# Performance work log

Measured on AMD Instinct MI355X. Metric: run time of the kernel, lower is better.

Reference implementation:

```python
import jax, jax.numpy as jnp
import numpy as np

D_MODEL = 1024
N_HEADS = 16
D_HEAD = D_MODEL // N_HEADS  # 64
NUM_MEM_KV = 4
SCALE = D_HEAD ** -0.5


def setup_inputs() -> dict:
    key = jax.random.key(0)
    k1, k2, k3, k4 = jax.random.split(key, 4)
    x = jax.random.normal(k1, (4, 4096, D_MODEL), dtype=jnp.float32)
    mask = jax.random.randint(k2, (4, 4096), 0, 2).astype(jnp.int32)
    w_qkv = jax.random.normal(k3, (3 * D_MODEL, D_MODEL), dtype=jnp.float32) * 0.02
    mem_kv = jax.random.normal(k4, (2, N_HEADS, NUM_MEM_KV, D_HEAD), dtype=jnp.float32)
    return {"x": x, "w_qkv": w_qkv, "mem_kv": mem_kv, "mask": mask}


def reference(x, w_qkv, mem_kv, mask):
    b, l, _ = x.shape
    # qkv projection: nn.Linear applies x @ W^T; reshape matches torch view(..., h, d_head, 3)
    qkv = jnp.einsum('bld,ed->ble', x, w_qkv).reshape(b, l, N_HEADS, D_HEAD, 3)
    qkv = jnp.moveaxis(qkv, 2, 1)  # (b, h, l, d_head, 3)
    q, k, v = qkv[..., 0], qkv[..., 1], qkv[..., 2]

    m = mask.astype(x.dtype)[:, None, :, None]  # (b, 1, l, 1) per prepare_mask
    k = jnp.where(m == 0, -jnp.inf, k * m)

    # prepend learned memory kv along the sequence axis
    mk = jnp.broadcast_to(mem_kv[0], (b, N_HEADS, NUM_MEM_KV, D_HEAD))
    mv = jnp.broadcast_to(mem_kv[1], (b, N_HEADS, NUM_MEM_KV, D_HEAD))
    k = jnp.concatenate([mk, k], axis=-2)  # (b, h, m+l, d_head)
    v = jnp.concatenate([mv, v], axis=-2)

    q = jax.nn.softmax(q * SCALE, axis=-1)   # softmax over feature dim
    k = jax.nn.softmax(k, axis=-2)           # softmax over sequence dim; -inf rows -> 0 weight

    context = jnp.einsum('bhnd,bhne->bhde', k, v)   # (b, h, d_head, d_head)
    out = jnp.einsum('bhld,bhde->bhle', q, context)  # (b, h, l, d_head)
    out = out * m
    out = jnp.moveaxis(out, 1, 2).reshape(b, l, N_HEADS * D_HEAD)
    return out
```

## Files before the change

kernel.cpp:

```cpp
#include <hip/hip_runtime.h>

typedef _Float16 h8 __attribute__((ext_vector_type(8)));
typedef _Float16 h4 __attribute__((ext_vector_type(4)));
typedef float f4 __attribute__((ext_vector_type(4)));

typedef __attribute__((address_space(1))) const void GV;
typedef __attribute__((address_space(3))) void SV;

__device__ __forceinline__ void async16(const void* g, void* s) {
  __builtin_amdgcn_global_load_lds((GV*)g, (SV*)s, 16, 0, 0);
}


#define XC 2097152
#define WC 393216

__global__ __launch_bounds__(256) void cvt_f16(const float4* __restrict__ x,
                                               const float4* __restrict__ w,
                                               h8* __restrict__ xh,
                                               h8* __restrict__ wh) {
  int t = blockIdx.x * 256 + threadIdx.x;
  if (t < XC) {
    const int row = t >> 7, c7 = t & 127;
    const int dst = (row << 7) | (c7 & 120) | ((c7 & 7) ^ (row & 7));
    float4 a = x[t * 2], b = x[t * 2 + 1];
    h8 o = {(_Float16)a.x, (_Float16)a.y, (_Float16)a.z, (_Float16)a.w,
            (_Float16)b.x, (_Float16)b.y, (_Float16)b.z, (_Float16)b.w};
    xh[dst] = o;
  } else {
    const int u = t - XC;
    const int rp = u >> 7, c7 = u & 127;
    int sr;
    if (rp < 2048) {
      int h = rp >> 7, c = rp & 127;
      sr = h * 192 + ((c < 64) ? (c * 3 + 1) : ((c - 64) * 3 + 2));
    } else {
      int q = rp - 2048;
      sr = (q >> 6) * 192 + (q & 63) * 3;
    }
    const int dst = (rp << 7) | (c7 & 120) | ((c7 & 7) ^ (rp & 7));
    float4 a = w[sr * 256 + c7 * 2], b = w[sr * 256 + c7 * 2 + 1];
    h8 o = {(_Float16)a.x, (_Float16)a.y, (_Float16)a.z, (_Float16)a.w,
            (_Float16)b.x, (_Float16)b.y, (_Float16)b.z, (_Float16)b.w};
    wh[dst] = o;
  }
}


__device__ __forceinline__ void ld4(h8 (&dst)[2][4], const _Float16* buf, int rbase,
                                    int l15, int quad, int swz) {
#pragma unroll
  for (int ks = 0; ks < 2; ++ks) {
    const int pc = ((((ks << 2) | quad) ^ swz)) << 3;
#pragma unroll
    for (int i = 0; i < 4; ++i)
      dst[ks][i] = *(const h8*)&buf[(rbase + i * 16 + l15) * 64 + pc];
  }
}

__device__ __forceinline__ void ld2(h8 (&dst)[2][2], const _Float16* buf, int rbase,
                                    int l15, int quad, int swz) {
#pragma unroll
  for (int ks = 0; ks < 2; ++ks) {
    const int pc = ((((ks << 2) | quad) ^ swz)) << 3;
#pragma unroll
    for (int j = 0; j < 2; ++j)
      dst[ks][j] = *(const h8*)&buf[(rbase + j * 16 + l15) * 64 + pc];
  }
}

template <int MH, int NH>
__device__ __forceinline__ void mq(f4 (&acc)[8][4], const h8 (&af)[2][4],
                                   const h8 (&bf)[2][2]) {
#pragma unroll
  for (int ks = 0; ks < 2; ++ks)
#pragma unroll
    for (int i = 0; i < 4; ++i)
#pragma unroll
      for (int j = 0; j < 2; ++j)
        acc[MH * 4 + i][NH * 2 + j] = __builtin_amdgcn_mfma_f32_16x16x32_f16(
            af[ks][i], bf[ks][j], acc[MH * 4 + i][NH * 2 + j], 0, 0, 0);
}

__device__ __forceinline__ void stage(const _Float16* g, _Float16* l, int it, int tid) {
  async16(g + (size_t)it * 65536, l + (it * 512 + tid) * 8);
}

__global__ __launch_bounds__(512, 2) void gemm_fused(const _Float16* __restrict__ A,
                                                     const _Float16* __restrict__ W,
                                                     const int* __restrict__ mask,
                                                     _Float16* __restrict__ P,
                                                     float* __restrict__ part) {
  __shared__ _Float16 smem[65536];
  _Float16* const As0 = smem;
  _Float16* const As1 = smem + 16384;
  _Float16* const Bs0 = smem + 32768;
  _Float16* const Bs1 = smem + 49152;
  const int tid = threadIdx.x;
  const int lane = tid & 63, wid = tid >> 6;
  const int wm = wid & 1, wn = wid >> 1;
  const int l15 = lane & 15, quad = lane >> 4;
  const int m0 = blockIdx.y * 256;
  const int n0 = blockIdx.x * 256;
  const int swz = l15 & 7;

  const int r0 = tid >> 3, cg = tid & 7;
  const _Float16* const Ab = A + (size_t)(m0 + r0) * 1024 + cg * 8;
  const _Float16* const Bb = W + (size_t)(n0 + r0) * 1024 + cg * 8;

  const f4 z = {0.f, 0.f, 0.f, 0.f};
  f4 acc[8][4];
#pragma unroll
  for (int i = 0; i < 8; ++i)
#pragma unroll
    for (int j = 0; j < 4; ++j) acc[i][j] = z;

#pragma unroll
  for (int it = 0; it < 4; ++it) {
    stage(Ab, As0, it, tid);
    stage(Bb, Bs0, it, tid);
  }
  stage(Ab + 64, As1, 0, tid);
  stage(Bb + 64, Bs1, 0, tid);
  stage(Ab + 64, As1, 1, tid);
  stage(Bb + 64, Bs1, 1, tid);
  asm volatile("s_waitcnt vmcnt(4)" ::: "memory");
  __builtin_amdgcn_s_barrier();

#pragma unroll 2
  for (int kt = 0; kt < 16; ++kt) {
    _Float16* const Ac = (kt & 1) ? As1 : As0;
    _Float16* const Bc = (kt & 1) ? Bs1 : Bs0;
    _Float16* const An = (kt & 1) ? As0 : As1;
    _Float16* const Bn = (kt & 1) ? Bs0 : Bs1;
    const _Float16* const Anx = Ab + (kt + 1) * 64;
    const _Float16* const Bnx = Bb + (kt + 1) * 64;
    h8 af[2][4], bf0[2][2], bf1[2][2];
    const int arb = wm * 128, brb = wn * 64;

    ld4(af, Ac, arb, l15, quad, swz);
    ld2(bf0, Bc, brb, l15, quad, swz);
    __builtin_amdgcn_s_barrier();
    asm volatile("s_waitcnt lgkmcnt(0)" ::: "memory");
    __builtin_amdgcn_s_setprio(1);
    mq<0, 0>(acc, af, bf0);
    __builtin_amdgcn_s_setprio(0);
    __builtin_amdgcn_s_barrier();

    ld2(bf1, Bc, brb + 32, l15, quad, swz);
    if (kt < 15) {
      stage(Anx, An, 2, tid);
      stage(Bnx, Bn, 2, tid);
    }
    __builtin_amdgcn_s_barrier();
    asm volatile("s_waitcnt lgkmcnt(0)" ::: "memory");
    __builtin_amdgcn_s_setprio(1);
    mq<0, 1>(acc, af, bf1);
    __builtin_amdgcn_s_setprio(0);
    __builtin_amdgcn_s_barrier();

    ld4(af, Ac, arb + 64, l15, quad, swz);
    __builtin_amdgcn_s_barrier();
    asm volatile("s_waitcnt lgkmcnt(0)" ::: "memory");
    __builtin_amdgcn_s_setprio(1);
    mq<1, 0>(acc, af, bf0);
    __builtin_amdgcn_s_setprio(0);
    __builtin_amdgcn_s_barrier();

    if (kt < 15) {
      stage(Anx, An, 3, tid);
      stage(Bnx, Bn, 3, tid);
    }
    __builtin_amdgcn_s_barrier();
    __builtin_amdgcn_s_setprio(1);
    mq<1, 1>(acc, af, bf1);
    __builtin_amdgcn_s_setprio(0);
    __builtin_amdgcn_s_barrier();

    if (kt < 14) {
      const _Float16* const A2 = Ab + (kt + 2) * 64;
      const _Float16* const B2 = Bb + (kt + 2) * 64;
      stage(A2, Ac, 0, tid);
      stage(B2, Bc, 0, tid);
      stage(A2, Ac, 1, tid);
      stage(B2, Bc, 1, tid);
      asm volatile("s_waitcnt vmcnt(4)" ::: "memory");
      __builtin_amdgcn_s_barrier();
    } else if (kt == 14) {
      asm volatile("s_waitcnt vmcnt(0)" ::: "memory");
      __builtin_amdgcn_s_barrier();
    }
  }

  if (n0 < 2048) {
    const int h0 = n0 >> 7;
    const int b = m0 >> 12;
    const int lc = (m0 & 4095) >> 8;
    const int hh = wn >> 1, isv = wn & 1;
#pragma unroll
    for (int i = 0; i < 8; ++i) {
      const int nb = wm * 128 + i * 16 + quad * 4;
      int mk[4];
      if (isv == 0) {
#pragma unroll
        for (int r = 0; r < 4; ++r) mk[r] = mask[m0 + nb + r];
      }
#pragma unroll
      for (int j = 0; j < 4; ++j) {
        const int cw = isv * 64 + j * 16 + l15;
        h4 o;
        if (isv == 0) {
#pragma unroll
          for (int r = 0; r < 4; ++r)
            o[r] = (_Float16)(mk[r] ? __expf(acc[i][j][r]) : 0.f);
        } else {
#pragma unroll
          for (int r = 0; r < 4; ++r) o[r] = (_Float16)acc[i][j][r];
        }
        *(h4*)&smem[(hh * 128 + cw) * 256 + (nb ^ (l15 * 8))] = o;
      }
    }
    __syncthreads();
    f4 cacc[5];
#pragma unroll
    for (int i = 0; i < 5; ++i) cacc[i] = z;
    h8 bones;
    {
      const _Float16 o1 = (l15 == 0) ? (_Float16)1.f : (_Float16)0.f;
#pragma unroll
      for (int j = 0; j < 8; ++j) bones[j] = o1;
    }
    const int hw = wid >> 2, dsw = (wid & 3) * 16;
    const _Float16* const hb = &smem[hw * 128 * 256];
#pragma unroll
    for (int ks = 0; ks < 8; ++ks) {
      const int nb2 = (ks * 32 + quad * 8) ^ (l15 * 8);
      h8 a = *(const h8*)&hb[(dsw + l15) * 256 + nb2];
#pragma unroll
      for (int et = 0; et < 4; ++et) {
        h8 bv = *(const h8*)&hb[(64 + et * 16 + l15) * 256 + nb2];
        cacc[et] = __builtin_amdgcn_mfma_f32_16x16x32_f16(a, bv, cacc[et], 0, 0, 0);
      }
      cacc[4] = __builtin_amdgcn_mfma_f32_16x16x32_f16(a, bones, cacc[4], 0, 0, 0);
    }
    const int bh = b * 16 + h0 + hw;
    const size_t pb = ((size_t)bh * 16 + lc) * 4160;
    const int dw = dsw + quad * 4;
#pragma unroll
    for (int et = 0; et < 4; ++et)
#pragma unroll
      for (int r = 0; r < 4; ++r)
        part[pb + (size_t)(dw + r) * 64 + et * 16 + l15] = cacc[et][r];
    if (l15 == 0) {
#pragma unroll
      for (int r = 0; r < 4; ++r) part[pb + 4096 + dw + r] = cacc[4][r];
    }
  } else {
    const int q0 = (n0 - 2048) + wn * 64;
#pragma unroll
    for (int i = 0; i < 8; ++i) {
      const int rg = m0 + wm * 128 + i * 16 + quad * 4;
#pragma unroll
      for (int j = 0; j < 4; ++j) {
        const int qc = q0 + j * 16 + l15;
#pragma unroll
        for (int r = 0; r < 4; ++r)
          P[(size_t)(rg + r) * 1024 + qc] = (_Float16)__expf(acc[i][j][r] * 0.125f);
      }
    }
  }
}

__global__ __launch_bounds__(256) void reduce_ctx(const float* __restrict__ part,
                                                  const float* __restrict__ memkv,
                                                  _Float16* __restrict__ ctxt) {
  const int bh = blockIdx.x;
  const int dsl = blockIdx.y;
  const int h = bh & 15;
  const int tid = threadIdx.x;
  const int dl = tid >> 6, e = tid & 63;
  const int d = dsl * 4 + dl;
  const size_t pb = (size_t)bh * 16 * 4160;

  float den = 0.f;
#pragma unroll 8
  for (int c = 0; c < 16; ++c) den += part[pb + (size_t)c * 4160 + 4096 + d];
  float s = 0.f;
#pragma unroll 8
  for (int c = 0; c < 16; ++c) s += part[pb + (size_t)c * 4160 + (size_t)d * 64 + e];
#pragma unroll
  for (int j = 0; j < 4; ++j) {
    const float ek = __expf(memkv[(h * 4 + j) * 64 + d]);
    den += ek;
    s += ek * memkv[4096 + (h * 4 + j) * 64 + e];
  }
  ctxt[(size_t)bh * 4096 + (size_t)e * 64 + d] = (_Float16)(s / den);
}

__global__ __launch_bounds__(256) void attn_out(const _Float16* __restrict__ P,
                                                const _Float16* __restrict__ ctxt,
                                                const int* __restrict__ mask,
                                                float* __restrict__ out) {
  const int l0 = blockIdx.x * 128;
  const int h = blockIdx.y;
  const int bh = (l0 >> 12) * 16 + h;
  const int tid = threadIdx.x;
  const int lane = tid & 63, wid = tid >> 6;
  const int l15 = lane & 15, quad = lane >> 4;

  h8 af[2][2], bf[2][4], bones;
  {
    const _Float16 o1 = (l15 == 0) ? (_Float16)1.f : (_Float16)0.f;
#pragma unroll
    for (int j = 0; j < 8; ++j) bones[j] = o1;
  }
#pragma unroll
  for (int i = 0; i < 2; ++i)
#pragma unroll
    for (int ks = 0; ks < 2; ++ks)
      af[i][ks] = *(const h8*)&P[(size_t)(l0 + wid * 32 + i * 16 + l15) * 1024 +
                                 h * 64 + ks * 32 + quad * 8];
#pragma unroll
  for (int ks = 0; ks < 2; ++ks)
#pragma unroll
    for (int et = 0; et < 4; ++et)
      bf[ks][et] = *(const h8*)&ctxt[(size_t)bh * 4096 +
                                     (size_t)(et * 16 + l15) * 64 + ks * 32 + quad * 8];

  const f4 z = {0.f, 0.f, 0.f, 0.f};
  f4 acc[2][5];
#pragma unroll
  for (int i = 0; i < 2; ++i)
#pragma unroll
    for (int j = 0; j < 5; ++j) acc[i][j] = z;
#pragma unroll
  for (int i = 0; i < 2; ++i)
#pragma unroll
    for (int ks = 0; ks < 2; ++ks) {
#pragma unroll
      for (int et = 0; et < 4; ++et)
        acc[i][et] = __builtin_amdgcn_mfma_f32_16x16x32_f16(af[i][ks], bf[ks][et], acc[i][et], 0, 0, 0);
      acc[i][4] = __builtin_amdgcn_mfma_f32_16x16x32_f16(af[i][ks], bones, acc[i][4], 0, 0, 0);
    }

#pragma unroll
  for (int i = 0; i < 2; ++i) {
#pragma unroll
    for (int r = 0; r < 4; ++r) {
      const int row = l0 + wid * 32 + i * 16 + quad * 4 + r;
      const float sb = __shfl(acc[i][4][r], lane & 48);
      const float iv = mask[row] ? 1.0f / sb : 0.0f;
#pragma unroll
      for (int et = 0; et < 4; ++et)
        out[(size_t)row * 1024 + h * 64 + et * 16 + l15] = acc[i][et][r] * iv;
    }
  }
}

extern "C" void kernel_launch(void* const* d_in, const int* in_sizes, int n_in,
                              void* d_out, int out_size, void* d_ws, size_t ws_size,
                              hipStream_t stream) {
  const float* x = (const float*)d_in[0];
  const float* w = (const float*)d_in[1];
  const float* memkv = (const float*)d_in[2];
  const int* mask = (const int*)d_in[3];
  float* out = (float*)d_out;

  char* ws = (char*)d_ws;
  _Float16* xh   = (_Float16*)(ws + 0);
  _Float16* wh   = (_Float16*)(ws + 33554432);
  _Float16* P    = (_Float16*)(ws + 39845888);
  float*    part = (float*)(ws + 73400320);
  _Float16* ctxt = (_Float16*)(ws + 107479040);

  cvt_f16<<<dim3(9728), dim3(256), 0, stream>>>((const float4*)x, (const float4*)w,
                                                (h8*)xh, (h8*)wh);
  gemm_fused<<<dim3(12, 64), dim3(512), 0, stream>>>(xh, wh, mask, P, part);
  reduce_ctx<<<dim3(64, 16), dim3(256), 0, stream>>>(part, memkv, ctxt);
  attn_out<<<dim3(128, 16), dim3(256), 0, stream>>>(P, ctxt, mask, out);
}
```

Measured before the change: 262.0 us.

## Prefetch full K-tile two steps ahead in GEMM double-buffer pipeline

Changes the GEMM main loop's global-to-LDS staging schedule. Previously the next tile was loaded in pieces across the iteration. Now the whole tile for step kt+2 is staged into the buffer just consumed: B is issued after its last read and A after the final A fragment load. This drops one barrier per iteration and gives loads a full iteration of lead time. In exchange it keeps more loads in flight, and correctness depends on the vmcnt and lgkmcnt wait counts being exactly right for the buffer reuse.

```diff
diff --git a/kernel.cpp b/kernel.cpp
--- a/kernel.cpp
+++ b/kernel.cpp
@@ -120,26 +120,26 @@
     stage(Ab, As0, it, tid);
     stage(Bb, Bs0, it, tid);
   }
-  stage(Ab + 64, As1, 0, tid);
-  stage(Bb + 64, Bs1, 0, tid);
-  stage(Ab + 64, As1, 1, tid);
-  stage(Bb + 64, Bs1, 1, tid);
-  asm volatile("s_waitcnt vmcnt(4)" ::: "memory");
+#pragma unroll
+  for (int it = 0; it < 4; ++it) {
+    stage(Ab + 64, As1, it, tid);
+    stage(Bb + 64, Bs1, it, tid);
+  }
+  asm volatile("s_waitcnt vmcnt(8)" ::: "memory");
   __builtin_amdgcn_s_barrier();
 
 #pragma unroll 2
   for (int kt = 0; kt < 16; ++kt) {
     _Float16* const Ac = (kt & 1) ? As1 : As0;
     _Float16* const Bc = (kt & 1) ? Bs1 : Bs0;
-    _Float16* const An = (kt & 1) ? As0 : As1;
-    _Float16* const Bn = (kt & 1) ? Bs0 : Bs1;
-    const _Float16* const Anx = Ab + (kt + 1) * 64;
-    const _Float16* const Bnx = Bb + (kt + 1) * 64;
+    const _Float16* const Ax2 = Ab + (kt + 2) * 64;
+    const _Float16* const Bx2 = Bb + (kt + 2) * 64;
     h8 af[2][4], bf0[2][2], bf1[2][2];
     const int arb = wm * 128, brb = wn * 64;
 
     ld4(af, Ac, arb, l15, quad, swz);
     ld2(bf0, Bc, brb, l15, quad, swz);
+    asm volatile("s_waitcnt lgkmcnt(8)" ::: "memory");
     __builtin_amdgcn_s_barrier();
     asm volatile("s_waitcnt lgkmcnt(0)" ::: "memory");
     __builtin_amdgcn_s_setprio(1);
@@ -148,10 +148,6 @@
     __builtin_amdgcn_s_barrier();
 
     ld2(bf1, Bc, brb + 32, l15, quad, swz);
-    if (kt < 15) {
-      stage(Anx, An, 2, tid);
-      stage(Bnx, Bn, 2, tid);
-    }
     __builtin_amdgcn_s_barrier();
     asm volatile("s_waitcnt lgkmcnt(0)" ::: "memory");
     __builtin_amdgcn_s_setprio(1);
@@ -160,6 +156,10 @@
     __builtin_amdgcn_s_barrier();
 
     ld4(af, Ac, arb + 64, l15, quad, swz);
+    if (kt < 14) {
+#pragma unroll
+      for (int it = 0; it < 4; ++it) stage(Bx2, Bc, it, tid);
+    }
     __builtin_amdgcn_s_barrier();
     asm volatile("s_waitcnt lgkmcnt(0)" ::: "memory");
     __builtin_amdgcn_s_setprio(1);
@@ -167,29 +167,20 @@
     __builtin_amdgcn_s_setprio(0);
     __builtin_amdgcn_s_barrier();
 
-    if (kt < 15) {
-      stage(Anx, An, 3, tid);
-      stage(Bnx, Bn, 3, tid);
+    if (kt < 14) {
+#pragma unroll
+      for (int it = 0; it < 4; ++it) stage(Ax2, Ac, it, tid);
     }
     __builtin_amdgcn_s_barrier();
     __builtin_amdgcn_s_setprio(1);
     mq<1, 1>(acc, af, bf1);
     __builtin_amdgcn_s_setprio(0);
-    __builtin_amdgcn_s_barrier();
-
     if (kt < 14) {
-      const _Float16* const A2 = Ab + (kt + 2) * 64;
-      const _Float16* const B2 = Bb + (kt + 2) * 64;
-      stage(A2, Ac, 0, tid);
-      stage(B2, Bc, 0, tid);
-      stage(A2, Ac, 1, tid);
-      stage(B2, Bc, 1, tid);
-      asm volatile("s_waitcnt vmcnt(4)" ::: "memory");
-      __builtin_amdgcn_s_barrier();
+      asm volatile("s_waitcnt vmcnt(8)" ::: "memory");
     } else if (kt == 14) {
       asm volatile("s_waitcnt vmcnt(0)" ::: "memory");
-      __builtin_amdgcn_s_barrier();
-    }
+    }
+    __builtin_amdgcn_s_barrier();
   }
 
   if (n0 < 2048) {
```

Measured after the change: 260.4 us. Within noise of the previous version (-0.6%).
